# Kernel optimization log

Hardware: AMD Instinct MI355X
Metric: run time of the kernel (lower is better)

## Reference

```python
import jax, jax.numpy as jnp
import numpy as np

B, N, C, H = 2, 2048, 768, 12
HD = C // H
SCALE = HD ** -0.5


def setup_inputs() -> dict:
    key = jax.random.key(0)
    k1, k2, k3, k4 = jax.random.split(key, 4)
    return {
        "x": jax.random.normal(k1, (B, N, C), dtype=jnp.float32),
        "qkv_w": jax.random.normal(k2, (3 * C, C), dtype=jnp.float32) * (C ** -0.5),
        "proj_w": jax.random.normal(k3, (C, C), dtype=jnp.float32) * (C ** -0.5),
        "proj_b": jax.random.normal(k4, (C,), dtype=jnp.float32) * 0.01,
    }


def reference(x, qkv_w, proj_w, proj_b):
    b, n, c = x.shape
    # qkv: Linear(dim, 3*dim, bias=False) -> (B,N,3,H,HD) -> per-tensor (B,H,N,HD)
    qkv = (x @ qkv_w.T).reshape(b, n, 3, H, HD)
    q, k, v = jnp.moveaxis(qkv, 2, 0)          # each (B,N,H,HD)
    q = q.transpose(0, 2, 1, 3)                # (B,H,N,HD)
    k = k.transpose(0, 2, 1, 3)
    v = v.transpose(0, 2, 1, 3)
    attn_logits = jnp.einsum("bhqd,bhkd->bhqk", q, k) * SCALE  # (B,H,N,N)
    attn = jax.nn.softmax(attn_logits, axis=-1)
    score = jnp.mean(attn, axis=1)             # (B,N,N) mean over heads
    # dropout p=0.0 -> identity
    out = jnp.einsum("bhqk,bhkd->bhqd", attn, v)  # (B,H,N,HD)
    out = out.transpose(0, 2, 1, 3).reshape(b, n, c)
    out = out @ proj_w.T + proj_b
    return out, score
```

## Files before the change

kernel.cpp:

```cpp
#include <hip/hip_runtime.h>
#include <cstddef>

typedef __attribute__((ext_vector_type(8))) short bf16x8;
typedef __attribute__((ext_vector_type(8))) short short8v;
typedef __attribute__((ext_vector_type(4))) float f32x4;
typedef __attribute__((ext_vector_type(16))) float f32x16;
typedef __attribute__((ext_vector_type(4))) unsigned u32x4;

constexpr int Bb = 2, Nn = 2048, Cc = 768, Hh = 12, HDd = 64;
constexpr int BHN = Bb * Hh * Nn;
constexpr size_t BNC = (size_t)Bb * Nn * Cc;
constexpr float QSCALE = 0.125f * 1.44269504088896340736f;

#define VMCNT(n) asm volatile("s_waitcnt vmcnt(" #n ")" ::: "memory")
#define SBAR() __builtin_amdgcn_s_barrier()

__device__ inline short f2bf(float f) {
  unsigned u = __builtin_bit_cast(unsigned, f);
  u += 0x7fff + ((u >> 16) & 1);
  return (short)(u >> 16);
}
__device__ inline float bf2f(short s) {
  unsigned u = ((unsigned)(unsigned short)s) << 16;
  return __builtin_bit_cast(float, u);
}
__device__ inline unsigned cvtpk(float a, float b) {
  unsigned r;
  asm("v_cvt_pk_bf16_f32 %0, %1, %2" : "=v"(r) : "v"(a), "v"(b));
  return r;
}
__device__ inline void pl32swap(unsigned& a, unsigned& b) {
  asm("v_permlane32_swap_b32 %0, %1" : "+v"(a), "+v"(b));
}
__device__ inline void gl_lds16(const void* g, void* l) {
  __builtin_amdgcn_global_load_lds(
      (const __attribute__((address_space(1))) unsigned*)g,
      (__attribute__((address_space(3))) unsigned*)l, 16, 0, 0);
}
__device__ inline bf16x8 lds8(const short* p) { return *(const bf16x8*)p; }
__device__ inline bf16x8 mk8(unsigned a, unsigned b, unsigned c, unsigned d) {
  u32x4 t = {a, b, c, d};
  return __builtin_bit_cast(bf16x8, t);
}
__device__ inline f32x16 zero16() {
  f32x16 z;
#pragma unroll
  for (int r = 0; r < 16; ++r) z[r] = 0.f;
  return z;
}
__device__ inline bf16x8 ld_frag(const short* base, int row, int ch) {
  return *(const bf16x8*)&base[row * 64 + (((ch ^ (row & 7)) << 3))];
}

__global__ __launch_bounds__(256) void cvt_kernel(const float* __restrict__ s,
                                                  short* __restrict__ d) {
  const int i = (blockIdx.x * 256 + threadIdx.x) * 4;
  const float4 v = *(const float4*)&s[i];
  short4 o;
  o.x = f2bf(v.x); o.y = f2bf(v.y); o.z = f2bf(v.z); o.w = f2bf(v.w);
  *(short4*)&d[i] = o;
}

__global__ __launch_bounds__(256) void qkv_mfma(
    const short* __restrict__ A, const short* __restrict__ W,
    short* __restrict__ Qg, short* __restrict__ Kg, short* __restrict__ Vtg) {
  __shared__ short As[2 * 8192];
  __shared__ short Bs[2 * 8192];
  const int t = threadIdx.x, l = t & 63, w = t >> 6;
  const int lr = l & 15, lh = l >> 4;
  const int m0 = blockIdx.x * 128, r0 = blockIdx.y * 128;
  const int wr = w >> 1, wc = w & 1;
  f32x4 acc[4][4];
#pragma unroll
  for (int i = 0; i < 4; ++i)
#pragma unroll
    for (int j = 0; j < 4; ++j) acc[i][j] = (f32x4){0.f, 0.f, 0.f, 0.f};

  auto stage = [&](const int buf, const int kt) {
#pragma unroll
    for (int u = 0; u < 4; ++u) {
      const int du = (w * 4 + u) * 64 + l;
      const int row = du >> 3, ch = du & 7, sch = ch ^ (row & 7);
      gl_lds16(A + (size_t)(m0 + row) * Cc + kt * 64 + sch * 8,
               &As[buf * 8192 + (w * 4 + u) * 512]);
      gl_lds16(W + (size_t)(r0 + row) * Cc + kt * 64 + sch * 8,
               &Bs[buf * 8192 + (w * 4 + u) * 512]);
    }
  };
  auto compute = [&](const int buf) {
    const short* Ab = As + buf * 8192;
    const short* Bbp = Bs + buf * 8192;
#pragma unroll
    for (int kp = 0; kp < 2; ++kp) {
      bf16x8 af[4], bfv[4];
#pragma unroll
      for (int i = 0; i < 4; ++i)
        af[i] = ld_frag(Ab, wr * 64 + i * 16 + lr, kp * 4 + lh);
#pragma unroll
      for (int j = 0; j < 4; ++j)
        bfv[j] = ld_frag(Bbp, wc * 64 + j * 16 + lr, kp * 4 + lh);
      __builtin_amdgcn_s_setprio(1);
#pragma unroll
      for (int i = 0; i < 4; ++i)
#pragma unroll
        for (int j = 0; j < 4; ++j)
          acc[i][j] = __builtin_amdgcn_mfma_f32_16x16x32_bf16(
              af[i], bfv[j], acc[i][j], 0, 0, 0);
      __builtin_amdgcn_s_setprio(0);
    }
  };

  stage(0, 0);
#pragma unroll 1
  for (int kk = 0; kk < 10; kk += 2) {
    stage(1, kk + 1);
    VMCNT(8); SBAR();
    compute(0);
    SBAR();
    stage(0, kk + 2);
    VMCNT(8); SBAR();
    compute(1);
    SBAR();
  }
  stage(1, 11);
  VMCNT(8); SBAR();
  compute(0);
  SBAR();
  VMCNT(0); SBAR();
  compute(1);

  const int which = r0 / Cc;
  const int rbase = r0 % Cc;
  const int bq = m0 >> 11;
  const int nb = (m0 & 2047) + wr * 64;
  if (which == 2) {
#pragma unroll
    for (int j = 0; j < 4; ++j) {
      const int rr = rbase + wc * 64 + j * 16 + lr;
      const int head = rr >> 6, dd = rr & 63;
      short* vp = &Vtg[(((size_t)bq * Hh + head) * HDd + dd) * Nn];
#pragma unroll
      for (int i = 0; i < 4; ++i) {
        short4 o;
        o.x = f2bf(acc[i][j][0]); o.y = f2bf(acc[i][j][1]);
        o.z = f2bf(acc[i][j][2]); o.w = f2bf(acc[i][j][3]);
        *(short4*)&vp[nb + i * 16 + lh * 4] = o;
      }
    }
  } else {
    const float scl = (which == 0) ? QSCALE : 1.0f;
    short* __restrict__ dst = (which == 0) ? Qg : Kg;
#pragma unroll
    for (int j = 0; j < 4; ++j) {
      const int rr = rbase + wc * 64 + j * 16 + lr;
      const int head = rr >> 6, dd = rr & 63;
      short* dp = &dst[((size_t)bq * Hh + head) * Nn * HDd + dd];
#pragma unroll
      for (int i = 0; i < 4; ++i)
#pragma unroll
        for (int r = 0; r < 4; ++r)
          dp[(size_t)(nb + i * 16 + lh * 4 + r) * HDd] =
              f2bf(acc[i][j][r] * scl);
    }
  }
}

__global__ __launch_bounds__(256, 3) void attn_pass1_split(
    const short* __restrict__ Qg, const short* __restrict__ Kg,
    const short* __restrict__ Vtg, float* __restrict__ Lpart,
    short* __restrict__ OHp) {
  __shared__ short SM[4 * 4096];
  const int t = threadIdx.x, l = t & 63, w = t >> 6;
  const int lo5 = l & 31, hi5 = l >> 5;
  const int raw = blockIdx.x;
  const int bid = (raw & 7) * 96 + (raw >> 3);
  const int split = bid & 1;
  const int qt = (bid >> 1) & 15;
  const int head = (bid >> 5) % Hh;
  const int b = (bid >> 5) / Hh;
  const size_t base = (size_t)b * Hh + head;
  const short* Qh = Qg + base * Nn * HDd;
  const short* Kh = Kg + base * Nn * HDd;
  const short* Vh = Vtg + base * HDd * Nn;
  const int qw = qt * 128 + w * 32;
  const int kvbase = split * 1024;

  int of2[2][4];
#pragma unroll
  for (int i = 0; i < 2; ++i)
#pragma unroll
    for (int s = 0; s < 4; ++s)
      of2[i][s] = (i * 32 + lo5) * 64 + ((((2 * s + hi5) ^ (l & 7))) << 3);

  bf16x8 qf[4];
#pragma unroll
  for (int s = 0; s < 4; ++s)
    qf[s] = *(const bf16x8*)&Qh[(size_t)(qw + lo5) * HDd + s * 16 + hi5 * 8];

  f32x16 accO0 = zero16(), accO1 = zero16();
  float Lp = 0.f;

  auto stage = [&](const int buf, const int tile) {
    const short* Kt = Kh + (size_t)(kvbase + tile * 64) * HDd;
    const short* Vt = Vh + kvbase + tile * 64;
#pragma unroll
    for (int u = 0; u < 2; ++u) {
      const int cu = u * 4 + w;
      const int du = cu * 64 + l;
      const int row = du >> 3, ch = du & 7, sch = ch ^ (row & 7);
      gl_lds16(Kt + row * 64 + sch * 8, &SM[buf * 4096 + cu * 512]);
      gl_lds16(Vt + (size_t)row * Nn + sch * 8,
               &SM[8192 + buf * 4096 + cu * 512]);
    }
  };

  auto compute = [&](const int kb) {
    const int vb = 8192 + kb;
    f32x16 s0 = zero16(), s1 = zero16();
    __builtin_amdgcn_s_setprio(1);
#pragma unroll
    for (int s = 0; s < 4; ++s)
      s0 = __builtin_amdgcn_mfma_f32_32x32x16_bf16(lds8(&SM[kb + of2[0][s]]),
                                                   qf[s], s0, 0, 0, 0);
#pragma unroll
    for (int s = 0; s < 4; ++s)
      s1 = __builtin_amdgcn_mfma_f32_32x32x16_bf16(lds8(&SM[kb + of2[1][s]]),
                                                   qf[s], s1, 0, 0, 0);
    __builtin_amdgcn_s_setprio(0);
    float p[16];
#pragma unroll
    for (int r = 0; r < 16; ++r) { p[r] = exp2f(s0[r]); Lp += p[r]; }
    unsigned a0 = cvtpk(p[0], p[1]), b0 = cvtpk(p[2], p[3]);
    unsigned c0 = cvtpk(p[4], p[5]), d0 = cvtpk(p[6], p[7]);
    pl32swap(a0, c0); pl32swap(b0, d0);
    const bf16x8 pa0 = mk8(a0, b0, c0, d0);
    unsigned a1 = cvtpk(p[8], p[9]), b1 = cvtpk(p[10], p[11]);
    unsigned c1 = cvtpk(p[12], p[13]), d1 = cvtpk(p[14], p[15]);
    pl32swap(a1, c1); pl32swap(b1, d1);
    const bf16x8 pa1 = mk8(a1, b1, c1, d1);
#pragma unroll
    for (int r = 0; r < 16; ++r) { p[r] = exp2f(s1[r]); Lp += p[r]; }
    unsigned a2 = cvtpk(p[0], p[1]), b2 = cvtpk(p[2], p[3]);
    unsigned c2 = cvtpk(p[4], p[5]), d2 = cvtpk(p[6], p[7]);
    pl32swap(a2, c2); pl32swap(b2, d2);
    const bf16x8 pa2 = mk8(a2, b2, c2, d2);
    unsigned a3 = cvtpk(p[8], p[9]), b3 = cvtpk(p[10], p[11]);
    unsigned c3 = cvtpk(p[12], p[13]), d3 = cvtpk(p[14], p[15]);
    pl32swap(a3, c3); pl32swap(b3, d3);
    const bf16x8 pa3 = mk8(a3, b3, c3, d3);
    __builtin_amdgcn_s_setprio(1);
    accO0 = __builtin_amdgcn_mfma_f32_32x32x16_bf16(lds8(&SM[vb + of2[0][0]]),
                                                    pa0, accO0, 0, 0, 0);
    accO1 = __builtin_amdgcn_mfma_f32_32x32x16_bf16(lds8(&SM[vb + of2[1][0]]),
                                                    pa0, accO1, 0, 0, 0);
    accO0 = __builtin_amdgcn_mfma_f32_32x32x16_bf16(lds8(&SM[vb + of2[0][1]]),
                                                    pa1, accO0, 0, 0, 0);
    accO1 = __builtin_amdgcn_mfma_f32_32x32x16_bf16(lds8(&SM[vb + of2[1][1]]),
                                                    pa1, accO1, 0, 0, 0);
    accO0 = __builtin_amdgcn_mfma_f32_32x32x16_bf16(lds8(&SM[vb + of2[0][2]]),
                                                    pa2, accO0, 0, 0, 0);
    accO1 = __builtin_amdgcn_mfma_f32_32x32x16_bf16(lds8(&SM[vb + of2[1][2]]),
                                                    pa2, accO1, 0, 0, 0);
    accO0 = __builtin_amdgcn_mfma_f32_32x32x16_bf16(lds8(&SM[vb + of2[0][3]]),
                                                    pa3, accO0, 0, 0, 0);
    accO1 = __builtin_amdgcn_mfma_f32_32x32x16_bf16(lds8(&SM[vb + of2[1][3]]),
                                                    pa3, accO1, 0, 0, 0);
    __builtin_amdgcn_s_setprio(0);
  };

  stage(0, 0);
#pragma unroll 1
  for (int it = 0; it < 14; it += 2) {
    stage(1, it + 1);
    VMCNT(4); SBAR();
    compute(0);
    SBAR();
    stage(0, it + 2);
    VMCNT(4); SBAR();
    compute(4096);
    SBAR();
  }
  stage(1, 15);
  VMCNT(4); SBAR();
  compute(0);
  SBAR();
  VMCNT(0); SBAR();
  compute(4096);

  Lp += __shfl_xor(Lp, 32);
  const int qv = qw + lo5;
  if (hi5 == 0) Lpart[(size_t)split * BHN + base * Nn + qv] = Lp;
  short* OHs = OHp + (size_t)split * BNC;
#pragma unroll
  for (int dh = 0; dh < 2; ++dh) {
#pragma unroll
    for (int g = 0; g < 4; ++g) {
      short4 o;
      if (dh == 0) {
        o.x = f2bf(accO0[4 * g + 0]); o.y = f2bf(accO0[4 * g + 1]);
        o.z = f2bf(accO0[4 * g + 2]); o.w = f2bf(accO0[4 * g + 3]);
      } else {
        o.x = f2bf(accO1[4 * g + 0]); o.y = f2bf(accO1[4 * g + 1]);
        o.z = f2bf(accO1[4 * g + 2]); o.w = f2bf(accO1[4 * g + 3]);
      }
      *(short4*)&OHs[((size_t)b * Nn + qv) * Cc + head * HDd + dh * 32 +
                     8 * g + 4 * hi5] = o;
    }
  }
}

__global__ __launch_bounds__(256) void combine_kernel(
    short* __restrict__ OHp, const float* __restrict__ Lpart,
    float* __restrict__ Linv) {
  const int tid = blockIdx.x * 256 + threadIdx.x;
  const int c8 = tid % 96;
  const int c = c8 * 8;
  const int mn = tid / 96;
  const int n = mn & 2047, b = mn >> 11;
  const int head = c >> 6;
  const int li = ((b * Hh + head) << 11) + n;
  const float lsum = Lpart[li] + Lpart[BHN + li];
  const float inv = 1.0f / lsum;
  const size_t off = (size_t)mn * Cc + c;
  const short8v o0 = *(const short8v*)&OHp[off];
  const short8v o1 = *(const short8v*)&OHp[BNC + off];
  short8v o;
#pragma unroll
  for (int e = 0; e < 8; ++e) o[e] = f2bf((bf2f(o0[e]) + bf2f(o1[e])) * inv);
  *(short8v*)&OHp[off] = o;
  if ((c & 63) == 0) Linv[li] = inv;
}

__global__ __launch_bounds__(256, 4) void score_mfma(
    const short* __restrict__ Qg, const short* __restrict__ Kg,
    const float* __restrict__ Linv, float* __restrict__ score) {
  __shared__ __align__(16) char SMraw[64 * 68 * 4];
  short* SK = (short*)SMraw;
  float* SMf = (float*)SMraw;
  const int t = threadIdx.x, l = t & 63, w = t >> 6;
  const int lr = l & 15, lh = l >> 4;
  const int raw = blockIdx.x;
  const int xcd = raw & 7, idx = raw >> 3;
  const int b = xcd >> 2;
  const int q0 = ((xcd & 3) * 8 + (idx >> 5)) * 64;
  const int kv0 = (idx & 31) * 64;
  const int qw = q0 + w * 16;

  int fof[2][4];
#pragma unroll
  for (int kp = 0; kp < 2; ++kp)
#pragma unroll
    for (int i = 0; i < 4; ++i)
      fof[kp][i] = (i * 16 + lr) * 64 + (((kp * 4 + lh) ^ (lr & 7)) << 3);

  f32x4 sc[4];
#pragma unroll
  for (int i = 0; i < 4; ++i) sc[i] = (f32x4){0.f, 0.f, 0.f, 0.f};

  auto stage = [&](const int kb, const int h) {
    const short* Kt = Kg + (((size_t)b * Hh + h) * Nn + kv0) * HDd;
#pragma unroll
    for (int u = 0; u < 2; ++u) {
      const int cu = u * 4 + w;
      const int du = cu * 64 + l;
      const int row = du >> 3, ch = du & 7, sch = ch ^ (row & 7);
      gl_lds16(Kt + row * 64 + sch * 8, &SK[kb + cu * 512]);
    }
  };
  auto ldqQ = [&](const int h, bf16x8& a0, bf16x8& a1) {
    const size_t hb = (size_t)b * Hh + h;
    a0 = *(const bf16x8*)&Qg[(hb * Nn + qw + lr) * HDd + lh * 8];
    a1 = *(const bf16x8*)&Qg[(hb * Nn + qw + lr) * HDd + 32 + lh * 8];
  };
  auto qk = [&](const int kb, const bf16x8 a0, const bf16x8 a1,
                f32x4 (&sacc)[4]) {
#pragma unroll
    for (int i = 0; i < 4; ++i) sacc[i] = (f32x4){0.f, 0.f, 0.f, 0.f};
#pragma unroll
    for (int i = 0; i < 4; ++i)
      sacc[i] = __builtin_amdgcn_mfma_f32_16x16x32_bf16(
          lds8(&SK[kb + fof[0][i]]), a0, sacc[i], 0, 0, 0);
#pragma unroll
    for (int i = 0; i < 4; ++i)
      sacc[i] = __builtin_amdgcn_mfma_f32_16x16x32_bf16(
          lds8(&SK[kb + fof[1][i]]), a1, sacc[i], 0, 0, 0);
  };
  auto expacc = [&](const f32x4 (&sacc)[4], const float lv) {
#pragma unroll
    for (int i = 0; i < 4; ++i)
#pragma unroll
      for (int r = 0; r < 4; ++r) sc[i][r] += exp2f(sacc[i][r]) * lv;
  };

  bf16x8 qA0, qA1, qB0, qB1;
  float lvA, lvB;
  f32x4 sA[4], sB[4];
  stage(0, 0);
  ldqQ(0, qA0, qA1);
  __syncthreads();
  stage(4096, 1);
  ldqQ(1, qB0, qB1);
  lvA = Linv[((size_t)b * Hh + 0) * Nn + qw + lr];
  qk(0, qA0, qA1, sA);
  __syncthreads();
#pragma unroll 1
  for (int h = 1; h < 11; h += 2) {
    stage(0, h + 1);
    ldqQ(h + 1, qA0, qA1);
    lvB = Linv[((size_t)b * Hh + h) * Nn + qw + lr];
    qk(4096, qB0, qB1, sB);
    expacc(sA, lvA);
    __syncthreads();
    stage(4096, h + 2);
    ldqQ(h + 2, qB0, qB1);
    lvA = Linv[((size_t)b * Hh + h + 1) * Nn + qw + lr];
    qk(0, qA0, qA1, sA);
    expacc(sB, lvB);
    __syncthreads();
  }
  lvB = Linv[((size_t)b * Hh + 11) * Nn + qw + lr];
  qk(4096, qB0, qB1, sB);
  expacc(sA, lvA);
  expacc(sB, lvB);
  __syncthreads();

  constexpr float invH = 1.0f / 12.0f;
#pragma unroll
  for (int i = 0; i < 4; ++i) {
    f32x4 o;
#pragma unroll
    for (int r = 0; r < 4; ++r) o[r] = sc[i][r] * invH;
    *(f32x4*)&SMf[(w * 16 + lr) * 68 + i * 16 + 4 * lh] = o;
  }
  __syncthreads();
#pragma unroll
  for (int s = 0; s < 4; ++s) {
    const int lin = t + s * 256;
    const int row = lin >> 4, ch = lin & 15;
    const f32x4 v = *(const f32x4*)&SMf[row * 68 + ch * 4];
    *(f32x4*)&score[((size_t)b * Nn + q0 + row) * Nn + kv0 + ch * 4] = v;
  }
}

__global__ __launch_bounds__(256) void proj_mfma(
    const short* __restrict__ A, const short* __restrict__ W,
    const float* __restrict__ bias, float* __restrict__ out) {
  __shared__ short As[128 * 64];
  __shared__ short Bs[128 * 64];
  const int t = threadIdx.x, l = t & 63, w = t >> 6;
  const int lr = l & 15, lh = l >> 4;
  const int m0 = blockIdx.x * 128, c0 = blockIdx.y * 128;
  const int wr = w >> 1, wc = w & 1;
  f32x4 acc[4][4];
#pragma unroll
  for (int i = 0; i < 4; ++i)
#pragma unroll
    for (int j = 0; j < 4; ++j) acc[i][j] = (f32x4){0.f, 0.f, 0.f, 0.f};

  for (int k0 = 0; k0 < Cc; k0 += 64) {
    __syncthreads();
#pragma unroll
    for (int u = 0; u < 4; ++u) {
      const int du = (w * 4 + u) * 64 + l;
      const int row = du >> 3, ch = du & 7, sch = ch ^ (row & 7);
      gl_lds16(A + (size_t)(m0 + row) * Cc + k0 + sch * 8,
               &As[(w * 4 + u) * 512]);
      gl_lds16(W + (size_t)(c0 + row) * Cc + k0 + sch * 8,
               &Bs[(w * 4 + u) * 512]);
    }
    __syncthreads();
#pragma unroll
    for (int kp = 0; kp < 2; ++kp) {
      bf16x8 af[4], bfv[4];
#pragma unroll
      for (int i = 0; i < 4; ++i)
        af[i] = ld_frag(As, wr * 64 + i * 16 + lr, kp * 4 + lh);
#pragma unroll
      for (int j = 0; j < 4; ++j)
        bfv[j] = ld_frag(Bs, wc * 64 + j * 16 + lr, kp * 4 + lh);
#pragma unroll
      for (int i = 0; i < 4; ++i)
#pragma unroll
        for (int j = 0; j < 4; ++j)
          acc[i][j] = __builtin_amdgcn_mfma_f32_16x16x32_bf16(
              af[i], bfv[j], acc[i][j], 0, 0, 0);
    }
  }
#pragma unroll
  for (int j = 0; j < 4; ++j) {
    const int c = c0 + wc * 64 + j * 16 + lr;
    const float bi = bias[c];
#pragma unroll
    for (int i = 0; i < 4; ++i)
#pragma unroll
      for (int r = 0; r < 4; ++r) {
        const int m = m0 + wr * 64 + i * 16 + lh * 4 + r;
        out[(size_t)m * Cc + c] = acc[i][j][r] + bi;
      }
  }
}

extern "C" void kernel_launch(void* const* d_in, const int* in_sizes, int n_in,
                              void* d_out, int out_size, void* d_ws,
                              size_t ws_size, hipStream_t stream) {
  const float* x = (const float*)d_in[0];
  const float* qkv_w = (const float*)d_in[1];
  const float* proj_w = (const float*)d_in[2];
  const float* proj_b = (const float*)d_in[3];

  float* out = (float*)d_out;
  float* score = out + BNC;

  const size_t nx = BNC;
  const size_t nwq = (size_t)3 * Cc * Cc;
  const size_t npw = (size_t)Cc * Cc;
  short* xb = (short*)d_ws;
  short* wqb = xb + nx;
  short* pwb = wqb + nwq;
  short* Qb = pwb + npw;
  short* Kb = Qb + nx;
  short* Vtb = Kb + nx;
  short* OHp = Vtb + nx;
  float* Lpart = (float*)(OHp + 2 * nx);
  float* Linv = Lpart + 2 * BHN;

  cvt_kernel<<<dim3((int)(nx / 1024)), 256, 0, stream>>>(x, xb);
  cvt_kernel<<<dim3((int)(nwq / 1024)), 256, 0, stream>>>(qkv_w, wqb);
  cvt_kernel<<<dim3((int)(npw / 1024)), 256, 0, stream>>>(proj_w, pwb);
  qkv_mfma<<<dim3(32, 18), 256, 0, stream>>>(xb, wqb, Qb, Kb, Vtb);
  attn_pass1_split<<<dim3(768), 256, 0, stream>>>(Qb, Kb, Vtb, Lpart, OHp);
  combine_kernel<<<dim3((int)(nx / 8 / 256)), 256, 0, stream>>>(OHp, Lpart,
                                                                Linv);
  score_mfma<<<dim3(2048), 256, 0, stream>>>(Qb, Kb, Linv, score);
  proj_mfma<<<dim3(32, 6), 256, 0, stream>>>(OHp, pwb, proj_b, out);
}
```

Baseline: 144.3 us.

## Enlarge per-wave query tiles in attention and score kernels, split KV four ways

The attention pass now gives each wave 64 query rows instead of 32 and splits the KV range into four parts instead of two. Each K/V tile loaded from LDS therefore feeds twice as many MFMAs. The score kernel likewise gives each wave 64 query rows with a 4x4 accumulator tile, cutting the grid from 2048 to 512 blocks and staging output through a smaller LDS buffer in two halves. The trade-offs are higher register pressure (launch bounds lowered to 2 blocks per SM), fewer blocks in the score kernel, and a combine step that now reads four partial buffers, one of which reuses the bf16 x workspace.

```diff
diff --git a/kernel.cpp b/kernel.cpp
--- a/kernel.cpp
+++ b/kernel.cpp
@@ -165,25 +165,26 @@
   }
 }
 
-__global__ __launch_bounds__(256, 3) void attn_pass1_split(
+__global__ __launch_bounds__(256, 2) void attn_pass1_split(
     const short* __restrict__ Qg, const short* __restrict__ Kg,
     const short* __restrict__ Vtg, float* __restrict__ Lpart,
-    short* __restrict__ OHp) {
+    short* __restrict__ P0, short* __restrict__ P1, short* __restrict__ P2,
+    short* __restrict__ P3) {
   __shared__ short SM[4 * 4096];
   const int t = threadIdx.x, l = t & 63, w = t >> 6;
   const int lo5 = l & 31, hi5 = l >> 5;
   const int raw = blockIdx.x;
   const int bid = (raw & 7) * 96 + (raw >> 3);
-  const int split = bid & 1;
-  const int qt = (bid >> 1) & 15;
+  const int split = bid & 3;
+  const int qt = (bid >> 2) & 7;
   const int head = (bid >> 5) % Hh;
   const int b = (bid >> 5) / Hh;
   const size_t base = (size_t)b * Hh + head;
   const short* Qh = Qg + base * Nn * HDd;
   const short* Kh = Kg + base * Nn * HDd;
   const short* Vh = Vtg + base * HDd * Nn;
-  const int qw = qt * 128 + w * 32;
-  const int kvbase = split * 1024;
+  const int qw = qt * 256 + w * 64;
+  const int kvbase = split * 512;
 
   int of2[2][4];
 #pragma unroll
@@ -192,13 +193,20 @@
     for (int s = 0; s < 4; ++s)
       of2[i][s] = (i * 32 + lo5) * 64 + ((((2 * s + hi5) ^ (l & 7))) << 3);
 
-  bf16x8 qf[4];
-#pragma unroll
-  for (int s = 0; s < 4; ++s)
-    qf[s] = *(const bf16x8*)&Qh[(size_t)(qw + lo5) * HDd + s * 16 + hi5 * 8];
-
-  f32x16 accO0 = zero16(), accO1 = zero16();
-  float Lp = 0.f;
+  bf16x8 qfA[4], qfB[4];
+#pragma unroll
+  for (int s = 0; s < 4; ++s) {
+    qfA[s] = *(const bf16x8*)&Qh[(size_t)(qw + lo5) * HDd + s * 16 + hi5 * 8];
+    qfB[s] =
+        *(const bf16x8*)&Qh[(size_t)(qw + 32 + lo5) * HDd + s * 16 + hi5 * 8];
+  }
+
+  f32x16 accO[2][2];
+#pragma unroll
+  for (int i = 0; i < 2; ++i)
+#pragma unroll
+    for (int j = 0; j < 2; ++j) accO[i][j] = zero16();
+  float LpA = 0.f, LpB = 0.f;
 
   auto stage = [&](const int buf, const int tile) {
     const short* Kt = Kh + (size_t)(kvbase + tile * 64) * HDd;
@@ -214,63 +222,80 @@
     }
   };
 
-  auto compute = [&](const int kb) {
-    const int vb = 8192 + kb;
-    f32x16 s0 = zero16(), s1 = zero16();
-    __builtin_amdgcn_s_setprio(1);
-#pragma unroll
-    for (int s = 0; s < 4; ++s)
-      s0 = __builtin_amdgcn_mfma_f32_32x32x16_bf16(lds8(&SM[kb + of2[0][s]]),
-                                                   qf[s], s0, 0, 0, 0);
-#pragma unroll
-    for (int s = 0; s < 4; ++s)
-      s1 = __builtin_amdgcn_mfma_f32_32x32x16_bf16(lds8(&SM[kb + of2[1][s]]),
-                                                   qf[s], s1, 0, 0, 0);
-    __builtin_amdgcn_s_setprio(0);
+  auto exppack = [&](const f32x16& s, bf16x8& plo, bf16x8& phi, float& Lp) {
     float p[16];
 #pragma unroll
-    for (int r = 0; r < 16; ++r) { p[r] = exp2f(s0[r]); Lp += p[r]; }
+    for (int r = 0; r < 16; ++r) { p[r] = exp2f(s[r]); Lp += p[r]; }
     unsigned a0 = cvtpk(p[0], p[1]), b0 = cvtpk(p[2], p[3]);
     unsigned c0 = cvtpk(p[4], p[5]), d0 = cvtpk(p[6], p[7]);
     pl32swap(a0, c0); pl32swap(b0, d0);
-    const bf16x8 pa0 = mk8(a0, b0, c0, d0);
+    plo = mk8(a0, b0, c0, d0);
     unsigned a1 = cvtpk(p[8], p[9]), b1 = cvtpk(p[10], p[11]);
     unsigned c1 = cvtpk(p[12], p[13]), d1 = cvtpk(p[14], p[15]);
     pl32swap(a1, c1); pl32swap(b1, d1);
-    const bf16x8 pa1 = mk8(a1, b1, c1, d1);
-#pragma unroll
-    for (int r = 0; r < 16; ++r) { p[r] = exp2f(s1[r]); Lp += p[r]; }
-    unsigned a2 = cvtpk(p[0], p[1]), b2 = cvtpk(p[2], p[3]);
-    unsigned c2 = cvtpk(p[4], p[5]), d2 = cvtpk(p[6], p[7]);
-    pl32swap(a2, c2); pl32swap(b2, d2);
-    const bf16x8 pa2 = mk8(a2, b2, c2, d2);
-    unsigned a3 = cvtpk(p[8], p[9]), b3 = cvtpk(p[10], p[11]);
-    unsigned c3 = cvtpk(p[12], p[13]), d3 = cvtpk(p[14], p[15]);
-    pl32swap(a3, c3); pl32swap(b3, d3);
-    const bf16x8 pa3 = mk8(a3, b3, c3, d3);
+    phi = mk8(a1, b1, c1, d1);
+  };
+
+  auto compute = [&](const int kb) {
+    const int vb = 8192 + kb;
+    f32x16 s00 = zero16(), s01 = zero16(), s10 = zero16(), s11 = zero16();
     __builtin_amdgcn_s_setprio(1);
-    accO0 = __builtin_amdgcn_mfma_f32_32x32x16_bf16(lds8(&SM[vb + of2[0][0]]),
-                                                    pa0, accO0, 0, 0, 0);
-    accO1 = __builtin_amdgcn_mfma_f32_32x32x16_bf16(lds8(&SM[vb + of2[1][0]]),
-                                                    pa0, accO1, 0, 0, 0);
-    accO0 = __builtin_amdgcn_mfma_f32_32x32x16_bf16(lds8(&SM[vb + of2[0][1]]),
-                                                    pa1, accO0, 0, 0, 0);
-    accO1 = __builtin_amdgcn_mfma_f32_32x32x16_bf16(lds8(&SM[vb + of2[1][1]]),
-                                                    pa1, accO1, 0, 0, 0);
-    accO0 = __builtin_amdgcn_mfma_f32_32x32x16_bf16(lds8(&SM[vb + of2[0][2]]),
-                                                    pa2, accO0, 0, 0, 0);
-    accO1 = __builtin_amdgcn_mfma_f32_32x32x16_bf16(lds8(&SM[vb + of2[1][2]]),
-                                                    pa2, accO1, 0, 0, 0);
-    accO0 = __builtin_amdgcn_mfma_f32_32x32x16_bf16(lds8(&SM[vb + of2[0][3]]),
-                                                    pa3, accO0, 0, 0, 0);
-    accO1 = __builtin_amdgcn_mfma_f32_32x32x16_bf16(lds8(&SM[vb + of2[1][3]]),
-                                                    pa3, accO1, 0, 0, 0);
+#pragma unroll
+    for (int s = 0; s < 4; ++s) {
+      const bf16x8 kf = lds8(&SM[kb + of2[0][s]]);
+      s00 = __builtin_amdgcn_mfma_f32_32x32x16_bf16(kf, qfA[s], s00, 0, 0, 0);
+      s01 = __builtin_amdgcn_mfma_f32_32x32x16_bf16(kf, qfB[s], s01, 0, 0, 0);
+    }
+#pragma unroll
+    for (int s = 0; s < 4; ++s) {
+      const bf16x8 kf = lds8(&SM[kb + of2[1][s]]);
+      s10 = __builtin_amdgcn_mfma_f32_32x32x16_bf16(kf, qfA[s], s10, 0, 0, 0);
+      s11 = __builtin_amdgcn_mfma_f32_32x32x16_bf16(kf, qfB[s], s11, 0, 0, 0);
+    }
+    __builtin_amdgcn_s_setprio(0);
+    bf16x8 paA0, paA1, paA2, paA3, paB0, paB1, paB2, paB3;
+    exppack(s00, paA0, paA1, LpA);
+    exppack(s10, paA2, paA3, LpA);
+    exppack(s01, paB0, paB1, LpB);
+    exppack(s11, paB2, paB3, LpB);
+    __builtin_amdgcn_s_setprio(1);
+#pragma unroll
+    for (int dh = 0; dh < 2; ++dh) {
+      {
+        const bf16x8 vf = lds8(&SM[vb + of2[dh][0]]);
+        accO[dh][0] = __builtin_amdgcn_mfma_f32_32x32x16_bf16(vf, paA0,
+                                                              accO[dh][0], 0, 0, 0);
+        accO[dh][1] = __builtin_amdgcn_mfma_f32_32x32x16_bf16(vf, paB0,
+                                                              accO[dh][1], 0, 0, 0);
+      }
+      {
+        const bf16x8 vf = lds8(&SM[vb + of2[dh][1]]);
+        accO[dh][0] = __builtin_amdgcn_mfma_f32_32x32x16_bf16(vf, paA1,
+                                                              accO[dh][0], 0, 0, 0);
+        accO[dh][1] = __builtin_amdgcn_mfma_f32_32x32x16_bf16(vf, paB1,
+                                                              accO[dh][1], 0, 0, 0);
+      }
+      {
+        const bf16x8 vf = lds8(&SM[vb + of2[dh][2]]);
+        accO[dh][0] = __builtin_amdgcn_mfma_f32_32x32x16_bf16(vf, paA2,
+                                                              accO[dh][0], 0, 0, 0);
+        accO[dh][1] = __builtin_amdgcn_mfma_f32_32x32x16_bf16(vf, paB2,
+                                                              accO[dh][1], 0, 0, 0);
+      }
+      {
+        const bf16x8 vf = lds8(&SM[vb + of2[dh][3]]);
+        accO[dh][0] = __builtin_amdgcn_mfma_f32_32x32x16_bf16(vf, paA3,
+                                                              accO[dh][0], 0, 0, 0);
+        accO[dh][1] = __builtin_amdgcn_mfma_f32_32x32x16_bf16(vf, paB3,
+                                                              accO[dh][1], 0, 0, 0);
+      }
+    }
     __builtin_amdgcn_s_setprio(0);
   };
 
   stage(0, 0);
 #pragma unroll 1
-  for (int it = 0; it < 14; it += 2) {
+  for (int it = 0; it < 6; it += 2) {
     stage(1, it + 1);
     VMCNT(4); SBAR();
     compute(0);
@@ -280,38 +305,41 @@
     compute(4096);
     SBAR();
   }
-  stage(1, 15);
+  stage(1, 7);
   VMCNT(4); SBAR();
   compute(0);
   SBAR();
   VMCNT(0); SBAR();
   compute(4096);
 
-  Lp += __shfl_xor(Lp, 32);
-  const int qv = qw + lo5;
-  if (hi5 == 0) Lpart[(size_t)split * BHN + base * Nn + qv] = Lp;
-  short* OHs = OHp + (size_t)split * BNC;
-#pragma unroll
-  for (int dh = 0; dh < 2; ++dh) {
-#pragma unroll
-    for (int g = 0; g < 4; ++g) {
-      short4 o;
-      if (dh == 0) {
-        o.x = f2bf(accO0[4 * g + 0]); o.y = f2bf(accO0[4 * g + 1]);
-        o.z = f2bf(accO0[4 * g + 2]); o.w = f2bf(accO0[4 * g + 3]);
-      } else {
-        o.x = f2bf(accO1[4 * g + 0]); o.y = f2bf(accO1[4 * g + 1]);
-        o.z = f2bf(accO1[4 * g + 2]); o.w = f2bf(accO1[4 * g + 3]);
-      }
-      *(short4*)&OHs[((size_t)b * Nn + qv) * Cc + head * HDd + dh * 32 +
-                     8 * g + 4 * hi5] = o;
+  LpA += __shfl_xor(LpA, 32);
+  LpB += __shfl_xor(LpB, 32);
+  short* OHs = (split == 0) ? P0 : (split == 1) ? P1 : (split == 2) ? P2 : P3;
+#pragma unroll
+  for (int qs = 0; qs < 2; ++qs) {
+    const int qv = qw + qs * 32 + lo5;
+    const float Lp = qs ? LpB : LpA;
+    if (hi5 == 0) Lpart[(size_t)split * BHN + base * Nn + qv] = Lp;
+#pragma unroll
+    for (int dh = 0; dh < 2; ++dh) {
+#pragma unroll
+      for (int g = 0; g < 4; ++g) {
+        short4 o;
+        o.x = f2bf(accO[dh][qs][4 * g + 0]);
+        o.y = f2bf(accO[dh][qs][4 * g + 1]);
+        o.z = f2bf(accO[dh][qs][4 * g + 2]);
+        o.w = f2bf(accO[dh][qs][4 * g + 3]);
+        *(short4*)&OHs[((size_t)b * Nn + qv) * Cc + head * HDd + dh * 32 +
+                       8 * g + 4 * hi5] = o;
+      }
     }
   }
 }
 
 __global__ __launch_bounds__(256) void combine_kernel(
-    short* __restrict__ OHp, const float* __restrict__ Lpart,
-    float* __restrict__ Linv) {
+    short* __restrict__ P0, const short* __restrict__ P1,
+    const short* __restrict__ P2, const short* __restrict__ P3,
+    const float* __restrict__ Lpart, float* __restrict__ Linv) {
   const int tid = blockIdx.x * 256 + threadIdx.x;
   const int c8 = tid % 96;
   const int c = c8 * 8;
@@ -319,32 +347,37 @@
   const int n = mn & 2047, b = mn >> 11;
   const int head = c >> 6;
   const int li = ((b * Hh + head) << 11) + n;
-  const float lsum = Lpart[li] + Lpart[BHN + li];
+  const float lsum = Lpart[li] + Lpart[BHN + li] + Lpart[2 * BHN + li] +
+                     Lpart[3 * BHN + li];
   const float inv = 1.0f / lsum;
   const size_t off = (size_t)mn * Cc + c;
-  const short8v o0 = *(const short8v*)&OHp[off];
-  const short8v o1 = *(const short8v*)&OHp[BNC + off];
+  const short8v o0 = *(const short8v*)&P0[off];
+  const short8v o1 = *(const short8v*)&P1[off];
+  const short8v o2 = *(const short8v*)&P2[off];
+  const short8v o3 = *(const short8v*)&P3[off];
   short8v o;
 #pragma unroll
-  for (int e = 0; e < 8; ++e) o[e] = f2bf((bf2f(o0[e]) + bf2f(o1[e])) * inv);
-  *(short8v*)&OHp[off] = o;
+  for (int e = 0; e < 8; ++e)
+    o[e] = f2bf((bf2f(o0[e]) + bf2f(o1[e]) + bf2f(o2[e]) + bf2f(o3[e])) * inv);
+  *(short8v*)&P0[off] = o;
   if ((c & 63) == 0) Linv[li] = inv;
 }
 
-__global__ __launch_bounds__(256, 4) void score_mfma(
+__global__ __launch_bounds__(256, 2) void score_mfma(
     const short* __restrict__ Qg, const short* __restrict__ Kg,
     const float* __restrict__ Linv, float* __restrict__ score) {
-  __shared__ __align__(16) char SMraw[64 * 68 * 4];
+  __shared__ __align__(16) char SMraw[256 * 36 * 4];
   short* SK = (short*)SMraw;
-  float* SMf = (float*)SMraw;
+  float* SOUT = (float*)SMraw;
   const int t = threadIdx.x, l = t & 63, w = t >> 6;
   const int lr = l & 15, lh = l >> 4;
   const int raw = blockIdx.x;
-  const int xcd = raw & 7, idx = raw >> 3;
-  const int b = xcd >> 2;
-  const int q0 = ((xcd & 3) * 8 + (idx >> 5)) * 64;
-  const int kv0 = (idx & 31) * 64;
-  const int qw = q0 + w * 16;
+  const int bid = (raw & 7) * 64 + (raw >> 3);
+  const int b = bid >> 8;
+  const int qt = (bid >> 5) & 7;
+  const int kv0 = (bid & 31) * 64;
+  const int q0 = qt * 256;
+  const int qw = q0 + w * 64;
 
   int fof[2][4];
 #pragma unroll
@@ -353,9 +386,11 @@
     for (int i = 0; i < 4; ++i)
       fof[kp][i] = (i * 16 + lr) * 64 + (((kp * 4 + lh) ^ (lr & 7)) << 3);
 
-  f32x4 sc[4];
-#pragma unroll
-  for (int i = 0; i < 4; ++i) sc[i] = (f32x4){0.f, 0.f, 0.f, 0.f};
+  f32x4 sc[4][4];
+#pragma unroll
+  for (int i = 0; i < 4; ++i)
+#pragma unroll
+    for (int j = 0; j < 4; ++j) sc[i][j] = (f32x4){0.f, 0.f, 0.f, 0.f};
 
   auto stage = [&](const int kb, const int h) {
     const short* Kt = Kg + (((size_t)b * Hh + h) * Nn + kv0) * HDd;
@@ -367,78 +402,79 @@
       gl_lds16(Kt + row * 64 + sch * 8, &SK[kb + cu * 512]);
     }
   };
-  auto ldqQ = [&](const int h, bf16x8& a0, bf16x8& a1) {
-    const size_t hb = (size_t)b * Hh + h;
-    a0 = *(const bf16x8*)&Qg[(hb * Nn + qw + lr) * HDd + lh * 8];
-    a1 = *(const bf16x8*)&Qg[(hb * Nn + qw + lr) * HDd + 32 + lh * 8];
-  };
-  auto qk = [&](const int kb, const bf16x8 a0, const bf16x8 a1,
-                f32x4 (&sacc)[4]) {
-#pragma unroll
-    for (int i = 0; i < 4; ++i) sacc[i] = (f32x4){0.f, 0.f, 0.f, 0.f};
-#pragma unroll
-    for (int i = 0; i < 4; ++i)
-      sacc[i] = __builtin_amdgcn_mfma_f32_16x16x32_bf16(
-          lds8(&SK[kb + fof[0][i]]), a0, sacc[i], 0, 0, 0);
-#pragma unroll
-    for (int i = 0; i < 4; ++i)
-      sacc[i] = __builtin_amdgcn_mfma_f32_16x16x32_bf16(
-          lds8(&SK[kb + fof[1][i]]), a1, sacc[i], 0, 0, 0);
-  };
-  auto expacc = [&](const f32x4 (&sacc)[4], const float lv) {
-#pragma unroll
-    for (int i = 0; i < 4; ++i)
-#pragma unroll
-      for (int r = 0; r < 4; ++r) sc[i][r] += exp2f(sacc[i][r]) * lv;
-  };
-
-  bf16x8 qA0, qA1, qB0, qB1;
-  float lvA, lvB;
-  f32x4 sA[4], sB[4];
+
+  bf16x8 qf[2][4];
+  float lv[4];
+
   stage(0, 0);
-  ldqQ(0, qA0, qA1);
-  __syncthreads();
-  stage(4096, 1);
-  ldqQ(1, qB0, qB1);
-  lvA = Linv[((size_t)b * Hh + 0) * Nn + qw + lr];
-  qk(0, qA0, qA1, sA);
   __syncthreads();
 #pragma unroll 1
-  for (int h = 1; h < 11; h += 2) {
-    stage(0, h + 1);
-    ldqQ(h + 1, qA0, qA1);
-    lvB = Linv[((size_t)b * Hh + h) * Nn + qw + lr];
-    qk(4096, qB0, qB1, sB);
-    expacc(sA, lvA);
+  for (int h = 0; h < Hh; ++h) {
+    if (h + 1 < Hh) stage(((h + 1) & 1) * 4096, h + 1);
+    const size_t hb = (size_t)b * Hh + h;
+#pragma unroll
+    for (int j = 0; j < 4; ++j) {
+      qf[0][j] = *(const bf16x8*)&Qg[(hb * Nn + qw + j * 16 + lr) * HDd +
+                                     lh * 8];
+      qf[1][j] = *(const bf16x8*)&Qg[(hb * Nn + qw + j * 16 + lr) * HDd + 32 +
+                                     lh * 8];
+      lv[j] = Linv[hb * Nn + qw + j * 16 + lr];
+    }
+    const int kb = (h & 1) * 4096;
+#pragma unroll
+    for (int ih = 0; ih < 4; ih += 2) {
+      f32x4 sacc[2][4];
+#pragma unroll
+      for (int ii = 0; ii < 2; ++ii)
+#pragma unroll
+        for (int j = 0; j < 4; ++j) sacc[ii][j] = (f32x4){0.f, 0.f, 0.f, 0.f};
+      __builtin_amdgcn_s_setprio(1);
+#pragma unroll
+      for (int kp = 0; kp < 2; ++kp)
+#pragma unroll
+        for (int ii = 0; ii < 2; ++ii) {
+          const bf16x8 kf = lds8(&SK[kb + fof[kp][ih + ii]]);
+#pragma unroll
+          for (int j = 0; j < 4; ++j)
+            sacc[ii][j] = __builtin_amdgcn_mfma_f32_16x16x32_bf16(
+                kf, qf[kp][j], sacc[ii][j], 0, 0, 0);
+        }
+      __builtin_amdgcn_s_setprio(0);
+#pragma unroll
+      for (int ii = 0; ii < 2; ++ii)
+#pragma unroll
+        for (int j = 0; j < 4; ++j)
+#pragma unroll
+          for (int r = 0; r < 4; ++r)
+            sc[ih + ii][j][r] += exp2f(sacc[ii][j][r]) * lv[j];
+    }
     __syncthreads();
-    stage(4096, h + 2);
-    ldqQ(h + 2, qB0, qB1);
-    lvA = Linv[((size_t)b * Hh + h + 1) * Nn + qw + lr];
-    qk(0, qA0, qA1, sA);
-    expacc(sB, lvB);
+  }
+
+  constexpr float invH = 1.0f / 12.0f;
+#pragma unroll 1
+  for (int h0 = 0; h0 < 2; ++h0) {
+#pragma unroll
+    for (int ii = 0; ii < 2; ++ii)
+#pragma unroll
+      for (int j = 0; j < 4; ++j) {
+        const int i = h0 * 2 + ii;
+        f32x4 o;
+#pragma unroll
+        for (int r = 0; r < 4; ++r) o[r] = sc[i][j][r] * invH;
+        const int ql = w * 64 + j * 16 + lr;
+        *(f32x4*)&SOUT[ql * 36 + ii * 16 + 4 * lh] = o;
+      }
     __syncthreads();
-  }
-  lvB = Linv[((size_t)b * Hh + 11) * Nn + qw + lr];
-  qk(4096, qB0, qB1, sB);
-  expacc(sA, lvA);
-  expacc(sB, lvB);
-  __syncthreads();
-
-  constexpr float invH = 1.0f / 12.0f;
-#pragma unroll
-  for (int i = 0; i < 4; ++i) {
-    f32x4 o;
-#pragma unroll
-    for (int r = 0; r < 4; ++r) o[r] = sc[i][r] * invH;
-    *(f32x4*)&SMf[(w * 16 + lr) * 68 + i * 16 + 4 * lh] = o;
-  }
-  __syncthreads();
-#pragma unroll
-  for (int s = 0; s < 4; ++s) {
-    const int lin = t + s * 256;
-    const int row = lin >> 4, ch = lin & 15;
-    const f32x4 v = *(const f32x4*)&SMf[row * 68 + ch * 4];
-    *(f32x4*)&score[((size_t)b * Nn + q0 + row) * Nn + kv0 + ch * 4] = v;
+#pragma unroll
+    for (int s = 0; s < 8; ++s) {
+      const int unit = s * 256 + t;
+      const int row = unit >> 3, u8 = unit & 7;
+      const f32x4 v = *(const f32x4*)&SOUT[row * 36 + u8 * 4];
+      *(f32x4*)&score[((size_t)b * Nn + q0 + row) * Nn + kv0 + h0 * 32 +
+                      u8 * 4] = v;
+    }
+    __syncthreads();
   }
 }
 
@@ -520,17 +556,21 @@
   short* Qb = pwb + npw;
   short* Kb = Qb + nx;
   short* Vtb = Kb + nx;
-  short* OHp = Vtb + nx;
-  float* Lpart = (float*)(OHp + 2 * nx);
-  float* Linv = Lpart + 2 * BHN;
+  short* OH = Vtb + nx;
+  short* P2 = OH + nx;
+  short* P3 = P2 + nx;
+  float* Lpart = (float*)(P3 + nx);
+  float* Linv = Lpart + 4 * BHN;
+  short* P1 = xb;
 
   cvt_kernel<<<dim3((int)(nx / 1024)), 256, 0, stream>>>(x, xb);
   cvt_kernel<<<dim3((int)(nwq / 1024)), 256, 0, stream>>>(qkv_w, wqb);
   cvt_kernel<<<dim3((int)(npw / 1024)), 256, 0, stream>>>(proj_w, pwb);
   qkv_mfma<<<dim3(32, 18), 256, 0, stream>>>(xb, wqb, Qb, Kb, Vtb);
-  attn_pass1_split<<<dim3(768), 256, 0, stream>>>(Qb, Kb, Vtb, Lpart, OHp);
-  combine_kernel<<<dim3((int)(nx / 8 / 256)), 256, 0, stream>>>(OHp, Lpart,
-                                                                Linv);
-  score_mfma<<<dim3(2048), 256, 0, stream>>>(Qb, Kb, Linv, score);
-  proj_mfma<<<dim3(32, 6), 256, 0, stream>>>(OHp, pwb, proj_b, out);
-}
+  attn_pass1_split<<<dim3(768), 256, 0, stream>>>(Qb, Kb, Vtb, Lpart, OH, P1,
+                                                  P2, P3);
+  combine_kernel<<<dim3((int)(nx / 8 / 256)), 256, 0, stream>>>(OH, P1, P2, P3,
+                                                                Lpart, Linv);
+  score_mfma<<<dim3(512), 256, 0, stream>>>(Qb, Kb, Linv, score);
+  proj_mfma<<<dim3(32, 6), 256, 0, stream>>>(OH, pwb, proj_b, out);
+}
```

Measured after the change: 197.2 us. +36.7%, slower.
